# Kernel tuning notes

Measured on AMD Instinct MI355X. Metric: run time of the kernel, lower is better.

Reference implementation:

```python
import jax, jax.numpy as jnp
import numpy as np

K_F = 3          # propagation kernel
PAD_F = 1
NUM = K_F * K_F - 1   # 8 non-reference neighbors
IDX_REF = NUM // 2    # 4
PROP_TIME = 18
B, H, W = 4, 240, 1216


def _conv2d_same(x, w, b):
    # x: (B,Cin,H,W), w: (Cout,Cin,kh,kw)
    y = jax.lax.conv_general_dilated(x, w, (1, 1), 'SAME',
                                     dimension_numbers=('NCHW', 'OIHW', 'NCHW'))
    return y + b[None, :, None, None]


def _bilinear(img, y, x):
    # img: (B,H,W); y,x: (B,K,H,W) float sample coords. Zero outside bounds (DCN semantics).
    Bv, Hv, Wv = img.shape
    flat = img.reshape(Bv, -1)
    y0 = jnp.floor(y)
    x0 = jnp.floor(x)
    wy = y - y0
    wx = x - x0

    def g(yy, xx):
        valid = (yy >= 0) & (yy <= Hv - 1) & (xx >= 0) & (xx <= Wv - 1)
        yc = jnp.clip(yy, 0, Hv - 1).astype(jnp.int32)
        xc = jnp.clip(xx, 0, Wv - 1).astype(jnp.int32)
        idx = (yc * Wv + xc).reshape(Bv, -1)
        v = jnp.take_along_axis(flat, idx, axis=1).reshape(yy.shape)
        return jnp.where(valid, v, jnp.zeros((), img.dtype))

    return ((1 - wy) * (1 - wx) * g(y0, x0)
            + (1 - wy) * wx * g(y0, x0 + 1)
            + wy * (1 - wx) * g(y1 := y0 + 1, x0)
            + wy * wx * g(y1, x0 + 1))


def _deform_agg(feat, off, mask, k, pad):
    # Modulated deformable conv with w == 1, b == 0, ch_f == 1.
    # feat: (B,1,H,W); off: (B,K,2,H,W) (dy,dx); mask: (B,K,H,W)
    Bv, _, Hv, Wv = feat.shape
    kk = jnp.arange(k)
    by = (jnp.repeat(kk, k) - pad).astype(feat.dtype)  # kernel base dy, row-major
    bx = (jnp.tile(kk, k) - pad).astype(feat.dtype)    # kernel base dx
    gy = jnp.arange(Hv, dtype=feat.dtype)[None, None, :, None]
    gx = jnp.arange(Wv, dtype=feat.dtype)[None, None, None, :]
    y = gy + by[None, :, None, None] + off[:, :, 0]
    x = gx + bx[None, :, None, None] + off[:, :, 1]
    s = _bilinear(feat[:, 0], y, x)                    # (B,K,H,W)
    return jnp.sum(s * mask, axis=1, keepdims=True)


def setup_inputs() -> dict:
    key = jax.random.key(0)
    k1, k2, k3, k4, k5, k6 = jax.random.split(key, 6)
    feat_init = jax.random.uniform(k1, (B, 1, H, W), jnp.float32)
    guidance = jax.random.normal(k2, (B, 8, H, W), jnp.float32)
    confidence = jax.random.uniform(k3, (B, 1, H, W), jnp.float32)
    dep = jax.random.uniform(k4, (B, 1, H, W), jnp.float32)
    valid = (jax.random.uniform(k5, (B, 1, H, W), jnp.float32) < 0.05)
    feat_fix = dep * valid.astype(jnp.float32)
    w_oa = 0.1 * jax.random.normal(k6, (3 * NUM, 8, 3, 3), jnp.float32)
    b_oa = jnp.zeros((3 * NUM,), jnp.float32)
    aff_scale_const = jnp.full((1,), 0.5 * NUM, jnp.float32)  # gamma * num (TGASS)
    return {'feat_init': feat_init, 'guidance': guidance, 'confidence': confidence,
            'feat_fix': feat_fix, 'w_oa': w_oa, 'b_oa': b_oa,
            'aff_scale_const': aff_scale_const}


def reference(feat_init, guidance, confidence, feat_fix, w_oa, b_oa, aff_scale_const):
    Bv, _, Hv, Wv = guidance.shape
    oa = _conv2d_same(guidance, w_oa, b_oa)                 # (B,24,H,W)
    o1, o2, aff = oa[:, :NUM], oa[:, NUM:2 * NUM], oa[:, 2 * NUM:]
    # torch: cat((o1,o2),1).view(B,num,2,H,W) then insert zero ref offset at idx_ref
    off = jnp.concatenate([o1, o2], axis=1).reshape(Bv, NUM, 2, Hv, Wv)
    zeros = jnp.zeros((Bv, 1, 2, Hv, Wv), off.dtype)
    off = jnp.concatenate([off[:, :IDX_REF], zeros, off[:, IDX_REF:]], axis=1)  # (B,9,2,H,W)

    # TGASS affinity
    aff = jnp.tanh(aff) / (aff_scale_const + 1e-8)          # (B,8,H,W)

    # confidence-weighted affinity: 1x1 deform-sample of confidence at each neighbor offset
    nbr = jnp.array([0, 1, 2, 3, 5, 6, 7, 8])
    off_c = jax.lax.stop_gradient(off[:, nbr])              # (B,8,2,H,W), offsets detached
    gy = jnp.arange(Hv, dtype=aff.dtype)[None, None, :, None]
    gx = jnp.arange(Wv, dtype=aff.dtype)[None, None, None, :]
    conf_aff = _bilinear(confidence[:, 0], gy + off_c[:, :, 0], gx + off_c[:, :, 1])
    aff = aff * conf_aff

    s = jnp.sum(jnp.abs(aff), axis=1, keepdims=True) + 1e-4
    s = jnp.maximum(s, 1.0)                                 # TGASS clamp
    aff = aff / s
    aff_ref = 1.0 - jnp.sum(aff, axis=1, keepdims=True)
    aff9 = jnp.concatenate([aff[:, :IDX_REF], aff_ref, aff[:, IDX_REF:]], axis=1)  # (B,9,H,W)

    # preserve_input mask
    mask_fix = (jnp.sum((feat_fix > 0.0).astype(feat_fix.dtype), axis=1, keepdims=True) > 0.0)
    mask_fix = jax.lax.stop_gradient(mask_fix.astype(feat_fix.dtype))

    def step(feat, _):
        feat = (1.0 - mask_fix) * feat + mask_fix * feat_fix
        feat = _deform_agg(feat, off, aff9, K_F, PAD_F)
        return feat, None

    feat_result, _ = jax.lax.scan(step, feat_init, None, length=PROP_TIME)
    return feat_result, off.reshape(Bv, -1, Hv, Wv), aff9
```

## Files before the change

kernel.cpp:

```cpp
#include <hip/hip_runtime.h>
#include <hip/hip_bf16.h>

#define B_ 4
#define H_ 240
#define W_ 1216
#define HW_ (H_*W_)
#define N1_ (B_*HW_)
#define PT_ 18

#define PR_ 4
#define TROWS2 (PR_ + 10)
#define TCOLS 274

__device__ __forceinline__ bool probe_bf16(const void* scale_ptr) {
    return ((const unsigned short*)scale_ptr)[0] == 0x4080;
}

template<bool BF>
__device__ __forceinline__ float ldT(const void* p, int i) {
    if (BF) {
        unsigned int u = (unsigned int)((const unsigned short*)p)[i];
        return __uint_as_float(u << 16);
    }
    return ((const float*)p)[i];
}

template<bool BF>
__device__ __forceinline__ void stT(void* p, int i, float v) {
    if (BF) ((__hip_bfloat16*)p)[i] = __float2bfloat16(v);
    else    ((float*)p)[i] = v;
}

__global__ __launch_bounds__(256) void k_prep_w(const void* __restrict__ w_oa,
                                                const void* __restrict__ b_oa,
                                                const void* __restrict__ scale,
                                                float* __restrict__ wc) {
    bool bf = probe_bf16(scale);
    int i = blockIdx.x * 256 + threadIdx.x;
    if (i < 1728) wc[i] = bf ? ldT<true>(w_oa, i) : ldT<false>(w_oa, i);
    if (i < 24)   wc[1728 + i] = bf ? ldT<true>(b_oa, i) : ldT<false>(b_oa, i);
}

__global__ __launch_bounds__(256) void k_init(const void* __restrict__ finit,
                                              const void* __restrict__ ffix,
                                              const void* __restrict__ scale,
                                              float* __restrict__ featA,
                                              float* __restrict__ featB,
                                              unsigned long long* __restrict__ mask64) {
    bool bf = probe_bf16(scale);
    int p = blockIdx.x * 256 + threadIdx.x;
    float fx = bf ? ldT<true>(ffix, p)  : ldT<false>(ffix, p);
    float fi = bf ? ldT<true>(finit, p) : ldT<false>(finit, p);
    bool fixed = fx > 0.0f;
    float v = fixed ? fx : fi;
    featA[p] = v;
    featB[p] = v;
    unsigned long long bal = __ballot(fixed);
    if ((threadIdx.x & 63) == 0) mask64[p >> 6] = bal;
}

template<bool BF>
__device__ __forceinline__ void conv_body(const void* __restrict__ guid,
                                          const void* __restrict__ conf,
                                          const void* __restrict__ scale,
                                          const float* __restrict__ wc,
                                          void* __restrict__ d_out,
                                          float* __restrict__ ws_off,
                                          float* __restrict__ ws_aff,
                                          int mode2) {
    int p = blockIdx.x * 256 + threadIdx.x;
    int b = p / HW_;
    int r = p - b * HW_;
    int h = r / W_;
    int w = r - h * W_;

    int idx0[9]; bool vld[9];
    #pragma unroll
    for (int t = 0; t < 9; ++t) {
        int hh = h + t / 3 - 1;
        int ww = w + t % 3 - 1;
        vld[t] = (hh >= 0) && (hh < H_) && (ww >= 0) && (ww < W_);
        idx0[t] = hh * W_ + ww;
    }

    float oa[24];
    #pragma unroll
    for (int co = 0; co < 24; ++co) oa[co] = wc[1728 + co];

    #pragma unroll
    for (int ci = 0; ci < 8; ++ci) {
        int cb = (b * 8 + ci) * HW_;
        float gv[9];
        #pragma unroll
        for (int t = 0; t < 9; ++t)
            gv[t] = vld[t] ? ldT<BF>(guid, cb + idx0[t]) : 0.0f;
        #pragma unroll
        for (int co = 0; co < 24; ++co)
            #pragma unroll
            for (int t = 0; t < 9; ++t)
                oa[co] = fmaf(gv[t], wc[(co * 8 + ci) * 9 + t], oa[co]);
    }

    float scl = ldT<BF>(scale, 0);
    float inv = 1.0f / (scl + 1e-8f);

    float aft[8];
    int cbase = b * HW_;
    #pragma unroll
    for (int t = 0; t < 8; ++t) {
        float a = tanhf(oa[16 + t]) * inv;
        float y = (float)h + oa[2 * t];
        float x = (float)w + oa[2 * t + 1];
        float y0f = floorf(y), x0f = floorf(x);
        int y0 = (int)y0f, x0 = (int)x0f;
        float wy = y - y0f, wx = x - x0f;
        int y0c = min(max(y0, 0), H_ - 1), y1c = min(max(y0 + 1, 0), H_ - 1);
        int x0c = min(max(x0, 0), W_ - 1), x1c = min(max(x0 + 1, 0), W_ - 1);
        bool vy0 = (y0 >= 0) && (y0 < H_), vy1 = (y0 >= -1) && (y0 < H_ - 1);
        bool vx0 = (x0 >= 0) && (x0 < W_), vx1 = (x0 >= -1) && (x0 < W_ - 1);
        float w00 = (1.0f - wy) * (1.0f - wx); w00 = (vy0 && vx0) ? w00 : 0.0f;
        float w01 = (1.0f - wy) * wx;          w01 = (vy0 && vx1) ? w01 : 0.0f;
        float w10 = wy * (1.0f - wx);          w10 = (vy1 && vx0) ? w10 : 0.0f;
        float w11 = wy * wx;                   w11 = (vy1 && vx1) ? w11 : 0.0f;
        float f00 = ldT<BF>(conf, cbase + y0c * W_ + x0c);
        float f01 = ldT<BF>(conf, cbase + y0c * W_ + x1c);
        float f10 = ldT<BF>(conf, cbase + y1c * W_ + x0c);
        float f11 = ldT<BF>(conf, cbase + y1c * W_ + x1c);
        float cv = w00 * f00 + w01 * f01 + w10 * f10 + w11 * f11;
        aft[t] = a * cv;
    }
    float s = 1e-4f;
    #pragma unroll
    for (int t = 0; t < 8; ++t) s += fabsf(aft[t]);
    s = fmaxf(s, 1.0f);
    float rs = 1.0f / s;
    float suma = 0.0f;
    #pragma unroll
    for (int t = 0; t < 8; ++t) { aft[t] *= rs; suma += aft[t]; }
    float aref = 1.0f - suma;

    #pragma unroll
    for (int t = 0; t < 8; ++t) {
        int n9 = t + (t >= 4 ? 1 : 0);
        stT<BF>(d_out, N1_ + (b * 18 + 2 * n9)     * HW_ + r, oa[2 * t]);
        stT<BF>(d_out, N1_ + (b * 18 + 2 * n9 + 1) * HW_ + r, oa[2 * t + 1]);
        stT<BF>(d_out, 19 * N1_ + (b * 9 + n9) * HW_ + r, aft[t]);
    }
    stT<BF>(d_out, N1_ + (b * 18 + 8) * HW_ + r, 0.0f);
    stT<BF>(d_out, N1_ + (b * 18 + 9) * HW_ + r, 0.0f);
    stT<BF>(d_out, 19 * N1_ + (b * 9 + 4) * HW_ + r, aref);

    if (BF && mode2) {
        #pragma unroll
        for (int t = 0; t < 8; ++t) {
            ws_off[t * N1_ + p]       = oa[2 * t];
            ws_off[(8 + t) * N1_ + p] = oa[2 * t + 1];
            int n9 = t + (t >= 4 ? 1 : 0);
            ws_aff[n9 * N1_ + p] = aft[t];
        }
        ws_aff[4 * N1_ + p] = aref;
    }
}

__global__ __launch_bounds__(256) void k_conv(const void* __restrict__ guid,
                                              const void* __restrict__ conf,
                                              const void* __restrict__ scale,
                                              const float* __restrict__ wc,
                                              void* __restrict__ d_out,
                                              float* __restrict__ ws_off,
                                              float* __restrict__ ws_aff,
                                              int mode2) {
    if (probe_bf16(scale))
        conv_body<true>(guid, conf, scale, wc, d_out, ws_off, ws_aff, mode2);
    else
        conv_body<false>(guid, conf, scale, wc, d_out, ws_off, ws_aff, mode2);
}

template<bool BF>
__device__ __forceinline__ void prop_body(float (*tile)[TCOLS],
                                          const float* __restrict__ src,
                                          float* __restrict__ dst,
                                          const float* __restrict__ ws_off,
                                          const float* __restrict__ ws_aff,
                                          const void* __restrict__ d_out_all,
                                          const unsigned long long* __restrict__ mask64,
                                          void* __restrict__ d_out_feat,
                                          int last, int mode2) {
    int tx = threadIdx.x;
    int bx = blockIdx.x;
    int h0 = blockIdx.y * PR_;
    int b  = blockIdx.z;
    int w  = bx * 256 + tx;
    bool active = (w < W_);
    bool use_ws = BF && (mode2 != 0);

    const float* sp = src + b * HW_;
    int row0 = h0 - 5;
    int col0 = bx * 256 - 8;

    for (int idx = tx; idx < TROWS2 * TCOLS; idx += 256) {
        int rr = idx / TCOLS;
        int cc = idx - rr * TCOLS;
        int gy = min(max(row0 + rr, 0), H_ - 1);
        int gx = min(max(col0 + cc, 0), W_ - 1);
        tile[rr][cc] = sp[gy * W_ + gx];
    }
    __syncthreads();
    if (!active) return;

    for (int ry = 0; ry < PR_; ++ry) {
        int h = h0 + ry;
        int r = h * W_ + w;
        int p = b * HW_ + r;

        float oy[8], ox[8], af[9];
        if (use_ws) {
            #pragma unroll
            for (int t = 0; t < 8; ++t) {
                oy[t] = ws_off[t * N1_ + p];
                ox[t] = ws_off[(8 + t) * N1_ + p];
            }
            #pragma unroll
            for (int n = 0; n < 9; ++n) af[n] = ws_aff[n * N1_ + p];
        } else {
            #pragma unroll
            for (int t = 0; t < 8; ++t) {
                int n9 = t + (t >= 4 ? 1 : 0);
                oy[t] = ldT<BF>(d_out_all, N1_ + (b * 18 + 2 * n9)     * HW_ + r);
                ox[t] = ldT<BF>(d_out_all, N1_ + (b * 18 + 2 * n9 + 1) * HW_ + r);
            }
            #pragma unroll
            for (int n = 0; n < 9; ++n)
                af[n] = ldT<BF>(d_out_all, 19 * N1_ + (b * 9 + n) * HW_ + r);
        }

        float acc = af[4] * tile[5 + ry][tx + 8];

        #pragma unroll
        for (int t = 0; t < 8; ++t) {
            int n9 = t + (t >= 4 ? 1 : 0);
            float y = (float)(h + n9 / 3 - 1) + oy[t];
            float x = (float)(w + n9 % 3 - 1) + ox[t];
            float y0f = floorf(y), x0f = floorf(x);
            int y0 = (int)y0f, x0 = (int)x0f;
            float wy = y - y0f, wx = x - x0f;
            int y0c = min(max(y0, 0), H_ - 1), y1c = min(max(y0 + 1, 0), H_ - 1);
            int x0c = min(max(x0, 0), W_ - 1), x1c = min(max(x0 + 1, 0), W_ - 1);
            bool vy0 = (y0 >= 0) && (y0 < H_), vy1 = (y0 >= -1) && (y0 < H_ - 1);
            bool vx0 = (x0 >= 0) && (x0 < W_), vx1 = (x0 >= -1) && (x0 < W_ - 1);
            float w00 = (1.0f - wy) * (1.0f - wx); w00 = (vy0 && vx0) ? w00 : 0.0f;
            float w01 = (1.0f - wy) * wx;          w01 = (vy0 && vx1) ? w01 : 0.0f;
            float w10 = wy * (1.0f - wx);          w10 = (vy1 && vx0) ? w10 : 0.0f;
            float w11 = wy * wx;                   w11 = (vy1 && vx1) ? w11 : 0.0f;

            int sy0 = y0c - row0, sy1 = y1c - row0;
            int sx0 = x0c - col0, sx1 = x1c - col0;
            float f00, f01, f10, f11;
            if ((sy0 >= 0) && (sy1 <= TROWS2 - 1) && (sx0 >= 0) && (sx1 <= TCOLS - 1)) {
                f00 = tile[sy0][sx0];
                f01 = tile[sy0][sx1];
                f10 = tile[sy1][sx0];
                f11 = tile[sy1][sx1];
            } else {
                f00 = sp[y0c * W_ + x0c];
                f01 = sp[y0c * W_ + x1c];
                f10 = sp[y1c * W_ + x0c];
                f11 = sp[y1c * W_ + x1c];
            }
            float v = w00 * f00 + w01 * f01 + w10 * f10 + w11 * f11;
            acc = fmaf(af[n9], v, acc);
        }

        if (last) {
            stT<BF>(d_out_feat, p, acc);
        } else {
            unsigned long long bal = mask64[p >> 6];
            bool fixed = (bal >> (p & 63)) & 1ull;
            if (!fixed) dst[p] = acc;
        }
    }
}

__global__ __launch_bounds__(256) void k_prop(const float* __restrict__ src,
                                              float* __restrict__ dst,
                                              const float* __restrict__ ws_off,
                                              const float* __restrict__ ws_aff,
                                              const void* __restrict__ d_out_all,
                                              const unsigned long long* __restrict__ mask64,
                                              const void* __restrict__ scale,
                                              void* __restrict__ d_out_feat,
                                              int last, int mode2) {
    __shared__ float tile[TROWS2][TCOLS];
    if (probe_bf16(scale))
        prop_body<true>(tile, src, dst, ws_off, ws_aff, d_out_all, mask64,
                        d_out_feat, last, mode2);
    else
        prop_body<false>(tile, src, dst, ws_off, ws_aff, d_out_all, mask64,
                         d_out_feat, last, mode2);
}

extern "C" void kernel_launch(void* const* d_in, const int* in_sizes, int n_in,
                              void* d_out, int out_size, void* d_ws, size_t ws_size,
                              hipStream_t stream) {
    const void* feat_init  = d_in[0];
    const void* guidance   = d_in[1];
    const void* confidence = d_in[2];
    const void* feat_fix   = d_in[3];
    const void* w_oa       = d_in[4];
    const void* b_oa       = d_in[5];
    const void* scale      = d_in[6];

    float* wsf    = (float*)d_ws;
    float* featA  = wsf;
    float* featB  = wsf + N1_;
    float* wc     = wsf + 2 * (size_t)N1_;
    unsigned long long* mask64 =
        (unsigned long long*)(wsf + 2 * (size_t)N1_ + 2048);
    float* ws_off = wsf + 2 * (size_t)N1_ + 2048 + 36480;
    float* ws_aff = ws_off + 16 * (size_t)N1_;

    size_t need2 = ((size_t)27 * N1_ + 2048 + 36480) * sizeof(float);
    int mode2 = (ws_size >= need2) ? 1 : 0;

    int grid = N1_ / 256;
    hipLaunchKernelGGL(k_prep_w, dim3(7), dim3(256), 0, stream, w_oa, b_oa, scale, wc);
    hipLaunchKernelGGL(k_init, dim3(grid), dim3(256), 0, stream,
                       feat_init, feat_fix, scale, featA, featB, mask64);
    hipLaunchKernelGGL(k_conv, dim3(grid), dim3(256), 0, stream,
                       guidance, confidence, scale, wc, d_out, ws_off, ws_aff, mode2);

    float* a = featA;
    float* bbuf = featB;
    dim3 pgrid(5, H_ / PR_, B_);
    for (int it = 0; it < PT_; ++it) {
        int last = (it == PT_ - 1) ? 1 : 0;
        hipLaunchKernelGGL(k_prop, pgrid, dim3(256), 0, stream,
                           a, bbuf, ws_off, ws_aff, d_out, mask64, scale,
                           d_out, last, mode2);
        float* t = a; a = bbuf; bbuf = t;
    }
}
```

Baseline: 987.8 us.

## Stage confidence tile in LDS for conv bilinear sampling and reorder conv loops

```diff
diff --git a/kernel.cpp b/kernel.cpp
--- a/kernel.cpp
+++ b/kernel.cpp
@@ -8,9 +8,11 @@
 #define N1_ (B_*HW_)
 #define PT_ 18
 
+#define TROWS 11
+#define TCOLS 274
+
 #define PR_ 4
 #define TROWS2 (PR_ + 10)
-#define TCOLS 274
 
 __device__ __forceinline__ bool probe_bf16(const void* scale_ptr) {
     return ((const unsigned short*)scale_ptr)[0] == 0x4080;
@@ -60,7 +62,8 @@
 }
 
 template<bool BF>
-__device__ __forceinline__ void conv_body(const void* __restrict__ guid,
+__device__ __forceinline__ void conv_body(float (*ct)[TCOLS],
+                                          const void* __restrict__ guid,
                                           const void* __restrict__ conf,
                                           const void* __restrict__ scale,
                                           const float* __restrict__ wc,
@@ -68,44 +71,58 @@
                                           float* __restrict__ ws_off,
                                           float* __restrict__ ws_aff,
                                           int mode2) {
-    int p = blockIdx.x * 256 + threadIdx.x;
-    int b = p / HW_;
-    int r = p - b * HW_;
-    int h = r / W_;
-    int w = r - h * W_;
-
-    int idx0[9]; bool vld[9];
+    int tx = threadIdx.x;
+    int bx = blockIdx.x;
+    int h  = blockIdx.y;
+    int b  = blockIdx.z;
+    int w  = bx * 256 + tx;
+    bool active = (w < W_);
+
+    int row0 = h - 5;
+    int col0 = bx * 256 - 8;
+    int cbase = b * HW_;
+
+    for (int idx = tx; idx < TROWS * TCOLS; idx += 256) {
+        int rr = idx / TCOLS;
+        int cc = idx - rr * TCOLS;
+        int gy = min(max(row0 + rr, 0), H_ - 1);
+        int gx = min(max(col0 + cc, 0), W_ - 1);
+        ct[rr][cc] = ldT<BF>(conf, cbase + gy * W_ + gx);
+    }
+    __syncthreads();
+    if (!active) return;
+
+    int r = h * W_ + w;
+    int p = cbase + r;
+
+    float g[8][9];
     #pragma unroll
     for (int t = 0; t < 9; ++t) {
         int hh = h + t / 3 - 1;
         int ww = w + t % 3 - 1;
-        vld[t] = (hh >= 0) && (hh < H_) && (ww >= 0) && (ww < W_);
-        idx0[t] = hh * W_ + ww;
+        bool v = (hh >= 0) && (hh < H_) && (ww >= 0) && (ww < W_);
+        int idx0 = hh * W_ + ww;
+        #pragma unroll
+        for (int ci = 0; ci < 8; ++ci)
+            g[ci][t] = v ? ldT<BF>(guid, (b * 8 + ci) * HW_ + idx0) : 0.0f;
     }
 
     float oa[24];
     #pragma unroll
-    for (int co = 0; co < 24; ++co) oa[co] = wc[1728 + co];
-
-    #pragma unroll
-    for (int ci = 0; ci < 8; ++ci) {
-        int cb = (b * 8 + ci) * HW_;
-        float gv[9];
+    for (int co = 0; co < 24; ++co) {
+        float a = wc[1728 + co];
         #pragma unroll
-        for (int t = 0; t < 9; ++t)
-            gv[t] = vld[t] ? ldT<BF>(guid, cb + idx0[t]) : 0.0f;
-        #pragma unroll
-        for (int co = 0; co < 24; ++co)
+        for (int ci = 0; ci < 8; ++ci)
             #pragma unroll
             for (int t = 0; t < 9; ++t)
-                oa[co] = fmaf(gv[t], wc[(co * 8 + ci) * 9 + t], oa[co]);
+                a = fmaf(g[ci][t], wc[(co * 8 + ci) * 9 + t], a);
+        oa[co] = a;
     }
 
     float scl = ldT<BF>(scale, 0);
     float inv = 1.0f / (scl + 1e-8f);
 
     float aft[8];
-    int cbase = b * HW_;
     #pragma unroll
     for (int t = 0; t < 8; ++t) {
         float a = tanhf(oa[16 + t]) * inv;
@@ -122,10 +139,20 @@
         float w01 = (1.0f - wy) * wx;          w01 = (vy0 && vx1) ? w01 : 0.0f;
         float w10 = wy * (1.0f - wx);          w10 = (vy1 && vx0) ? w10 : 0.0f;
         float w11 = wy * wx;                   w11 = (vy1 && vx1) ? w11 : 0.0f;
-        float f00 = ldT<BF>(conf, cbase + y0c * W_ + x0c);
-        float f01 = ldT<BF>(conf, cbase + y0c * W_ + x1c);
-        float f10 = ldT<BF>(conf, cbase + y1c * W_ + x0c);
-        float f11 = ldT<BF>(conf, cbase + y1c * W_ + x1c);
+        int sy0 = y0c - row0, sy1 = y1c - row0;
+        int sx0 = x0c - col0, sx1 = x1c - col0;
+        float f00, f01, f10, f11;
+        if ((sy0 >= 0) && (sy1 <= TROWS - 1) && (sx0 >= 0) && (sx1 <= TCOLS - 1)) {
+            f00 = ct[sy0][sx0];
+            f01 = ct[sy0][sx1];
+            f10 = ct[sy1][sx0];
+            f11 = ct[sy1][sx1];
+        } else {
+            f00 = ldT<BF>(conf, cbase + y0c * W_ + x0c);
+            f01 = ldT<BF>(conf, cbase + y0c * W_ + x1c);
+            f10 = ldT<BF>(conf, cbase + y1c * W_ + x0c);
+            f11 = ldT<BF>(conf, cbase + y1c * W_ + x1c);
+        }
         float cv = w00 * f00 + w01 * f01 + w10 * f10 + w11 * f11;
         aft[t] = a * cv;
     }
@@ -170,10 +197,11 @@
                                               float* __restrict__ ws_off,
                                               float* __restrict__ ws_aff,
                                               int mode2) {
+    __shared__ float ct[TROWS][TCOLS];
     if (probe_bf16(scale))
-        conv_body<true>(guid, conf, scale, wc, d_out, ws_off, ws_aff, mode2);
+        conv_body<true>(ct, guid, conf, scale, wc, d_out, ws_off, ws_aff, mode2);
     else
-        conv_body<false>(guid, conf, scale, wc, d_out, ws_off, ws_aff, mode2);
+        conv_body<false>(ct, guid, conf, scale, wc, d_out, ws_off, ws_aff, mode2);
 }
 
 template<bool BF>
@@ -326,7 +354,7 @@
     hipLaunchKernelGGL(k_prep_w, dim3(7), dim3(256), 0, stream, w_oa, b_oa, scale, wc);
     hipLaunchKernelGGL(k_init, dim3(grid), dim3(256), 0, stream,
                        feat_init, feat_fix, scale, featA, featB, mask64);
-    hipLaunchKernelGGL(k_conv, dim3(grid), dim3(256), 0, stream,
+    hipLaunchKernelGGL(k_conv, dim3(5, H_, B_), dim3(256), 0, stream,
                        guidance, confidence, scale, wc, d_out, ws_off, ws_aff, mode2);
 
     float* a = featA;
```

After: 997.0 us. About the same (+0.9%).
